# Performance work log

Hardware: AMD Instinct MI355X
Metric: run time of the kernel (lower is better)

## Reference

```python
import jax, jax.numpy as jnp
import numpy as np

B, S, E, H = 8, 1024, 768, 12
D = E // H  # 64


def setup_inputs() -> dict:
    key = jax.random.key(0)
    ks = jax.random.split(key, 9)
    s = 0.02
    hidden_state = jax.random.normal(ks[0], (B, S, E), dtype=jnp.float32)
    # per-head projections stacked: [H, E, D]
    Wq = jax.random.normal(ks[1], (H, E, D), dtype=jnp.float32) * s
    Wk = jax.random.normal(ks[2], (H, E, D), dtype=jnp.float32) * s
    Wv = jax.random.normal(ks[3], (H, E, D), dtype=jnp.float32) * s
    bq = jax.random.normal(ks[4], (H, D), dtype=jnp.float32) * s
    bk = jax.random.normal(ks[5], (H, D), dtype=jnp.float32) * s
    bv = jax.random.normal(ks[6], (H, D), dtype=jnp.float32) * s
    Wo = jax.random.normal(ks[7], (E, E), dtype=jnp.float32) * s
    bo = jax.random.normal(ks[8], (E,), dtype=jnp.float32) * s
    return dict(hidden_state=hidden_state, Wq=Wq, Wk=Wk, Wv=Wv,
                bq=bq, bk=bk, bv=bv, Wo=Wo, bo=bo)


def reference(hidden_state, Wq, Wk, Wv, bq, bk, bv, Wo, bo):
    # project: [B,S,E] x [H,E,D] -> [B,H,S,D]
    q = jnp.einsum('bse,hed->bhsd', hidden_state, Wq) + bq[None, :, None, :]
    k = jnp.einsum('bse,hed->bhsd', hidden_state, Wk) + bk[None, :, None, :]
    v = jnp.einsum('bse,hed->bhsd', hidden_state, Wv) + bv[None, :, None, :]
    scale = 1.0 / jnp.sqrt(jnp.float32(D))
    scores = jnp.einsum('bhsd,bhtd->bhst', q, k) * scale  # [B,H,S,S]
    weights = jax.nn.softmax(scores, axis=-1)
    attn = jnp.einsum('bhst,bhtd->bhsd', weights, v)  # [B,H,S,D]
    # concat heads -> [B,S,E]
    x = attn.transpose(0, 2, 1, 3).reshape(B, S, E)
    return x @ Wo + bo
```

## Files before the change

kernel.cpp:

```cpp
#include <hip/hip_runtime.h>
#include <math.h>

#define BB 8
#define SS 1024
#define EE 768
#define HH 12
#define DD 64

typedef short bf16x8 __attribute__((ext_vector_type(8)));
typedef float f32x4  __attribute__((ext_vector_type(4)));
typedef unsigned short u16x4 __attribute__((ext_vector_type(4)));
typedef unsigned short u16x8 __attribute__((ext_vector_type(8)));

__device__ __forceinline__ unsigned short f2bf(float f) {
    union { float f; unsigned u; } v; v.f = f;
    unsigned r = v.u + 0x7fffu + ((v.u >> 16) & 1u);
    return (unsigned short)(r >> 16);
}

#define SWZ(row, byte) ((byte) ^ (((row) & 7) << 4))

__global__ __launch_bounds__(256) void conv_hs_kernel(
    const float* __restrict__ in, unsigned short* __restrict__ out)
{
    size_t i = ((size_t)blockIdx.x * 256 + threadIdx.x) * 8;
    float4 a = *reinterpret_cast<const float4*>(&in[i]);
    float4 b = *reinterpret_cast<const float4*>(&in[i + 4]);
    u16x8 o;
    o[0] = f2bf(a.x); o[1] = f2bf(a.y); o[2] = f2bf(a.z); o[3] = f2bf(a.w);
    o[4] = f2bf(b.x); o[5] = f2bf(b.y); o[6] = f2bf(b.z); o[7] = f2bf(b.w);
    *reinterpret_cast<u16x8*>(&out[i]) = o;
}

__global__ __launch_bounds__(256) void conv_wqkv_kernel(
    const float* __restrict__ Wq, const float* __restrict__ Wk,
    const float* __restrict__ Wv, unsigned short* __restrict__ WT)
{
    const int z = blockIdx.z;
    const int which = z / HH, h = z - which * HH;
    const float* in = ((which == 0) ? Wq : (which == 1) ? Wk : Wv) + (size_t)h * EE * DD;
    unsigned short* out = WT + (size_t)z * DD * EE;
    const float sc = (which == 0) ? 0.125f : 1.0f;

    __shared__ float t[64][65];
    const int tid = threadIdx.x;
    const int rt0 = blockIdx.x * 64;

    #pragma unroll
    for (int i = 0; i < 16; ++i) {
        int lin = tid + i * 256;
        int r = lin >> 6, c = lin & 63;
        t[r][c] = in[(size_t)(rt0 + r) * DD + c];
    }
    __syncthreads();
    #pragma unroll
    for (int i = 0; i < 16; ++i) {
        int lin = tid + i * 256;
        int c = lin >> 6, r = lin & 63;
        out[(size_t)c * EE + rt0 + r] = f2bf(t[r][c] * sc);
    }
}

__global__ __launch_bounds__(256) void conv_wo_kernel(
    const float* __restrict__ Wo, unsigned short* __restrict__ WoT)
{
    __shared__ float t[64][65];
    const int tid = threadIdx.x;
    const int rt0 = blockIdx.x * 64;
    const int ct0 = blockIdx.y * 64;

    #pragma unroll
    for (int i = 0; i < 16; ++i) {
        int lin = tid + i * 256;
        int r = lin >> 6, c = lin & 63;
        t[r][c] = Wo[(size_t)(rt0 + r) * EE + ct0 + c];
    }
    __syncthreads();
    #pragma unroll
    for (int i = 0; i < 16; ++i) {
        int lin = tid + i * 256;
        int c = lin >> 6, r = lin & 63;
        WoT[(size_t)(ct0 + c) * EE + rt0 + r] = f2bf(t[r][c]);
    }
}

__global__ __launch_bounds__(256) void qkv_mfma_kernel(
    const unsigned short* __restrict__ hsb, const unsigned short* __restrict__ WT,
    const float* __restrict__ bq, const float* __restrict__ bk, const float* __restrict__ bv,
    unsigned short* __restrict__ qo, unsigned short* __restrict__ ko,
    unsigned short* __restrict__ vto)
{
    __shared__ alignas(16) char As[128 * 128];
    __shared__ alignas(16) char Bs[64 * 128];

    const int tid = threadIdx.x;
    const int wv  = tid >> 6;
    const int ln  = tid & 63;
    const int g   = ln >> 4;
    const int lr  = ln & 15;
    const int r0    = blockIdx.x * 128;
    const int h     = blockIdx.y;
    const int which = blockIdx.z;

    const unsigned short* Wt = WT + (size_t)(which * HH + h) * DD * EE;
    const float* bias = (which == 0) ? bq : (which == 1) ? bk : bv;
    const float bsc   = (which == 0) ? 0.125f : 1.0f;

    f32x4 acc[2][4] = {};

    for (int k0 = 0; k0 < EE; k0 += 64) {
        __syncthreads();
        #pragma unroll
        for (int i = 0; i < 4; ++i) {
            int seg = tid + i * 256;
            int row = seg >> 3;
            int sb  = (seg & 7) * 16;
            *reinterpret_cast<bf16x8*>(As + SWZ(row, row * 128 + sb)) =
                *reinterpret_cast<const bf16x8*>(&hsb[(size_t)(r0 + row) * EE + k0 + (seg & 7) * 8]);
        }
        #pragma unroll
        for (int i = 0; i < 2; ++i) {
            int seg = tid + i * 256;
            int row = seg >> 3;
            int sb  = (seg & 7) * 16;
            *reinterpret_cast<bf16x8*>(Bs + SWZ(row, row * 128 + sb)) =
                *reinterpret_cast<const bf16x8*>(&Wt[(size_t)row * EE + k0 + (seg & 7) * 8]);
        }
        __syncthreads();

        #pragma unroll
        for (int c = 0; c < 2; ++c) {
            bf16x8 af[2];
            #pragma unroll
            for (int wr = 0; wr < 2; ++wr) {
                const int arow = wv * 32 + wr * 16 + lr;
                af[wr] = *reinterpret_cast<const bf16x8*>(
                    As + SWZ(arow, arow * 128 + c * 64 + g * 16));
            }
            #pragma unroll
            for (int nf = 0; nf < 4; ++nf) {
                const int bcol = nf * 16 + lr;
                bf16x8 bf = *reinterpret_cast<const bf16x8*>(
                    Bs + SWZ(bcol, bcol * 128 + c * 64 + g * 16));
                #pragma unroll
                for (int wr = 0; wr < 2; ++wr)
                    acc[wr][nf] = __builtin_amdgcn_mfma_f32_16x16x32_bf16(af[wr], bf, acc[wr][nf], 0, 0, 0);
            }
        }
    }

    if (which < 2) {
        unsigned short* C = (which == 0) ? qo : ko;
        #pragma unroll
        for (int nf = 0; nf < 4; ++nf) {
            const int d = nf * 16 + lr;
            const float bia = bias[h * DD + d] * bsc;
            #pragma unroll
            for (int wr = 0; wr < 2; ++wr)
                #pragma unroll
                for (int rr = 0; rr < 4; ++rr) {
                    int row = r0 + wv * 32 + wr * 16 + g * 4 + rr;
                    int b_ = row >> 10, s_ = row & 1023;
                    C[((size_t)(b_ * HH + h) * SS + s_) * DD + d] = f2bf(acc[wr][nf][rr] + bia);
                }
        }
    } else {
        #pragma unroll
        for (int nf = 0; nf < 4; ++nf) {
            const int d = nf * 16 + lr;
            const float bia = bias[h * DD + d];
            #pragma unroll
            for (int wr = 0; wr < 2; ++wr)
                #pragma unroll
                for (int rr = 0; rr < 4; ++rr) {
                    int row = r0 + wv * 32 + wr * 16 + g * 4 + rr;
                    int b_ = row >> 10, s_ = row & 1023;
                    vto[((size_t)(b_ * HH + h) * DD + d) * SS + s_] = f2bf(acc[wr][nf][rr] + bia);
                }
        }
    }
}

__global__ __launch_bounds__(256) void attn_mfma_kernel(
    const unsigned short* __restrict__ qb, const unsigned short* __restrict__ kb,
    const unsigned short* __restrict__ vtb, unsigned short* __restrict__ x)
{
    __shared__ alignas(16) char Ks[64 * 128];
    __shared__ alignas(16) char Vs[64 * 128];
    __shared__ alignas(16) char Pl[4 * 16 * 128];

    const int tid = threadIdx.x;
    const int wv  = tid >> 6;
    const int ln  = tid & 63;
    const int g   = ln >> 4;
    const int lr  = ln & 15;
    const int bh  = blockIdx.y;
    const int qw  = blockIdx.x * 64 + wv * 16;

    const size_t qrow = (size_t)(bh * SS + qw + lr) * DD;
    bf16x8 qf0 = *reinterpret_cast<const bf16x8*>(&qb[qrow + g * 8]);
    bf16x8 qf1 = *reinterpret_cast<const bf16x8*>(&qb[qrow + 32 + g * 8]);

    f32x4 acc_o[4] = {};
    f32x4 lrow = {};

    char* Pw = Pl + wv * 2048;

    for (int t0 = 0; t0 < SS; t0 += 64) {
        __syncthreads();
        #pragma unroll
        for (int i = 0; i < 2; ++i) {
            int c = tid + i * 256;
            int row = c >> 3;
            int seg = c & 7;
            *reinterpret_cast<bf16x8*>(Ks + SWZ(row, row * 128 + seg * 16)) =
                *reinterpret_cast<const bf16x8*>(&kb[(size_t)(bh * SS + t0 + row) * DD + seg * 8]);
            *reinterpret_cast<bf16x8*>(Vs + SWZ(row, row * 128 + seg * 16)) =
                *reinterpret_cast<const bf16x8*>(&vtb[(size_t)(bh * DD + row) * SS + t0 + seg * 8]);
        }
        __syncthreads();

        f32x4 s[4] = {};
        #pragma unroll
        for (int kf = 0; kf < 4; ++kf) {
            int key = kf * 16 + lr;
            bf16x8 k0 = *reinterpret_cast<const bf16x8*>(Ks + SWZ(key, key * 128 + g * 16));
            bf16x8 k1 = *reinterpret_cast<const bf16x8*>(Ks + SWZ(key, key * 128 + 64 + g * 16));
            s[kf] = __builtin_amdgcn_mfma_f32_16x16x32_bf16(qf0, k0, s[kf], 0, 0, 0);
            s[kf] = __builtin_amdgcn_mfma_f32_16x16x32_bf16(qf1, k1, s[kf], 0, 0, 0);
        }

        #pragma unroll
        for (int kf = 0; kf < 4; ++kf)
            #pragma unroll
            for (int r = 0; r < 4; ++r) {
                float p = __expf(s[kf][r]);
                s[kf][r] = p;
                lrow[r] += p;
            }

        #pragma unroll
        for (int kf = 0; kf < 4; ++kf)
            #pragma unroll
            for (int r = 0; r < 4; ++r) {
                int row = g * 4 + r;
                *reinterpret_cast<unsigned short*>(
                    Pw + SWZ(row, row * 128 + (kf * 16 + lr) * 2)) = f2bf(s[kf][r]);
            }

        #pragma unroll
        for (int kk = 0; kk < 2; ++kk) {
            bf16x8 pf8 = *reinterpret_cast<const bf16x8*>(
                Pw + SWZ(lr, lr * 128 + kk * 64 + g * 16));
            #pragma unroll
            for (int nf = 0; nf < 4; ++nf) {
                int d = nf * 16 + lr;
                bf16x8 vf8 = *reinterpret_cast<const bf16x8*>(
                    Vs + SWZ(d, d * 128 + kk * 64 + g * 16));
                acc_o[nf] = __builtin_amdgcn_mfma_f32_16x16x32_bf16(pf8, vf8, acc_o[nf], 0, 0, 0);
            }
        }
    }

    #pragma unroll
    for (int off = 1; off <= 8; off <<= 1)
        #pragma unroll
        for (int r = 0; r < 4; ++r) lrow[r] += __shfl_xor(lrow[r], off, 64);

    const int b_ = bh / HH;
    const int h_ = bh % HH;
    #pragma unroll
    for (int nf = 0; nf < 4; ++nf)
        #pragma unroll
        for (int r = 0; r < 4; ++r) {
            x[(size_t)(b_ * SS + qw + g * 4 + r) * EE + h_ * DD + nf * 16 + lr] =
                f2bf(acc_o[nf][r] / lrow[r]);
        }
}

__global__ __launch_bounds__(256) void out_mfma_kernel(
    const unsigned short* __restrict__ xb, const unsigned short* __restrict__ WoT,
    const float* __restrict__ bo, float* __restrict__ out)
{
    __shared__ alignas(16) char As[64 * 128];
    __shared__ alignas(16) char Bs[64 * 128];

    const int tid = threadIdx.x;
    const int wv  = tid >> 6;
    const int ln  = tid & 63;
    const int g   = ln >> 4;
    const int lr  = ln & 15;
    const int r0  = blockIdx.x * 64;
    const int c0  = blockIdx.y * 64;

    f32x4 acc[4] = {};

    for (int k0 = 0; k0 < EE; k0 += 64) {
        __syncthreads();
        #pragma unroll
        for (int i = 0; i < 2; ++i) {
            int seg = tid + i * 256;
            int row = seg >> 3;
            int sb  = (seg & 7) * 16;
            *reinterpret_cast<bf16x8*>(As + SWZ(row, row * 128 + sb)) =
                *reinterpret_cast<const bf16x8*>(&xb[(size_t)(r0 + row) * EE + k0 + (seg & 7) * 8]);
            *reinterpret_cast<bf16x8*>(Bs + SWZ(row, row * 128 + sb)) =
                *reinterpret_cast<const bf16x8*>(&WoT[(size_t)(c0 + row) * EE + k0 + (seg & 7) * 8]);
        }
        __syncthreads();

        #pragma unroll
        for (int c = 0; c < 2; ++c) {
            const int arow = wv * 16 + lr;
            bf16x8 af = *reinterpret_cast<const bf16x8*>(
                As + SWZ(arow, arow * 128 + c * 64 + g * 16));
            #pragma unroll
            for (int nf = 0; nf < 4; ++nf) {
                const int bcol = nf * 16 + lr;
                bf16x8 bf = *reinterpret_cast<const bf16x8*>(
                    Bs + SWZ(bcol, bcol * 128 + c * 64 + g * 16));
                acc[nf] = __builtin_amdgcn_mfma_f32_16x16x32_bf16(af, bf, acc[nf], 0, 0, 0);
            }
        }
    }

    #pragma unroll
    for (int nf = 0; nf < 4; ++nf) {
        const int d = c0 + nf * 16 + lr;
        const float bia = bo[d];
        #pragma unroll
        for (int rr = 0; rr < 4; ++rr) {
            int row = r0 + wv * 16 + g * 4 + rr;
            out[(size_t)row * EE + d] = acc[nf][rr] + bia;
        }
    }
}

extern "C" void kernel_launch(void* const* d_in, const int* in_sizes, int n_in,
                              void* d_out, int out_size, void* d_ws, size_t ws_size,
                              hipStream_t stream) {
    const float* hs = (const float*)d_in[0];
    const float* Wq = (const float*)d_in[1];
    const float* Wk = (const float*)d_in[2];
    const float* Wv = (const float*)d_in[3];
    const float* bq = (const float*)d_in[4];
    const float* bk = (const float*)d_in[5];
    const float* bv = (const float*)d_in[6];
    const float* Wo = (const float*)d_in[7];
    const float* bo = (const float*)d_in[8];
    float* out = (float*)d_out;

    const size_t per = (size_t)BB * HH * SS * DD;
    unsigned short* qb  = (unsigned short*)d_ws;
    unsigned short* kb  = qb + per;
    unsigned short* vtb = kb + per;
    unsigned short* xb  = vtb + per;
    unsigned short* hsb = xb + per;
    unsigned short* WT  = hsb + per;
    unsigned short* WoT = WT + (size_t)3 * HH * DD * EE;

    conv_hs_kernel<<<dim3(BB * SS * EE / 8 / 256), 256, 0, stream>>>(hs, hsb);
    conv_wqkv_kernel<<<dim3(EE / 64, 1, 3 * HH), 256, 0, stream>>>(Wq, Wk, Wv, WT);
    conv_wo_kernel<<<dim3(EE / 64, EE / 64), 256, 0, stream>>>(Wo, WoT);

    qkv_mfma_kernel<<<dim3(BB * SS / 128, HH, 3), 256, 0, stream>>>(
        hsb, WT, bq, bk, bv, qb, kb, vtb);

    attn_mfma_kernel<<<dim3(SS / 64, BB * HH), 256, 0, stream>>>(qb, kb, vtb, xb);

    out_mfma_kernel<<<dim3(BB * SS / 64, EE / 64), 256, 0, stream>>>(xb, WoT, bo, out);
}
```

Baseline: 237.9 us.

## Enlarge GEMM tiles to 128x128 and process 32 queries per wave in attention

The QKV and output projection kernels switch to 128x128 block tiles with a 2x2 wave grid and 4x4 MFMA accumulators per wave, so each LDS fragment load feeds more MFMAs. The attention kernel gives each wave two 16-row query groups, which halves the K/V tile loads per query and doubles LDS reuse. It also remaps the block index so consecutive blocks group heads per XCD for better L2 locality. In exchange, register and LDS use go up, which may reduce occupancy, and fewer blocks are launched.

```diff
diff --git a/kernel.cpp b/kernel.cpp
--- a/kernel.cpp
+++ b/kernel.cpp
@@ -9,7 +9,6 @@
 
 typedef short bf16x8 __attribute__((ext_vector_type(8)));
 typedef float f32x4  __attribute__((ext_vector_type(4)));
-typedef unsigned short u16x4 __attribute__((ext_vector_type(4)));
 typedef unsigned short u16x8 __attribute__((ext_vector_type(8)));
 
 __device__ __forceinline__ unsigned short f2bf(float f) {
@@ -91,22 +90,19 @@
     unsigned short* __restrict__ vto)
 {
     __shared__ alignas(16) char As[128 * 128];
-    __shared__ alignas(16) char Bs[64 * 128];
+    __shared__ alignas(16) char Bs[128 * 128];
 
     const int tid = threadIdx.x;
     const int wv  = tid >> 6;
     const int ln  = tid & 63;
     const int g   = ln >> 4;
     const int lr  = ln & 15;
-    const int r0    = blockIdx.x * 128;
-    const int h     = blockIdx.y;
-    const int which = blockIdx.z;
-
-    const unsigned short* Wt = WT + (size_t)(which * HH + h) * DD * EE;
-    const float* bias = (which == 0) ? bq : (which == 1) ? bk : bv;
-    const float bsc   = (which == 0) ? 0.125f : 1.0f;
-
-    f32x4 acc[2][4] = {};
+    const int wr  = wv >> 1;
+    const int wc  = wv & 1;
+    const int r0  = blockIdx.x * 128;
+    const int c0  = blockIdx.y * 128;
+
+    f32x4 acc[4][4] = {};
 
     for (int k0 = 0; k0 < EE; k0 += 64) {
         __syncthreads();
@@ -114,40 +110,40 @@
         for (int i = 0; i < 4; ++i) {
             int seg = tid + i * 256;
             int row = seg >> 3;
-            int sb  = (seg & 7) * 16;
-            *reinterpret_cast<bf16x8*>(As + SWZ(row, row * 128 + sb)) =
-                *reinterpret_cast<const bf16x8*>(&hsb[(size_t)(r0 + row) * EE + k0 + (seg & 7) * 8]);
-        }
-        #pragma unroll
-        for (int i = 0; i < 2; ++i) {
-            int seg = tid + i * 256;
-            int row = seg >> 3;
-            int sb  = (seg & 7) * 16;
-            *reinterpret_cast<bf16x8*>(Bs + SWZ(row, row * 128 + sb)) =
-                *reinterpret_cast<const bf16x8*>(&Wt[(size_t)row * EE + k0 + (seg & 7) * 8]);
+            int ch  = seg & 7;
+            *reinterpret_cast<bf16x8*>(As + SWZ(row, row * 128 + ch * 16)) =
+                *reinterpret_cast<const bf16x8*>(&hsb[(size_t)(r0 + row) * EE + k0 + ch * 8]);
+            *reinterpret_cast<bf16x8*>(Bs + SWZ(row, row * 128 + ch * 16)) =
+                *reinterpret_cast<const bf16x8*>(&WT[(size_t)(c0 + row) * EE + k0 + ch * 8]);
         }
         __syncthreads();
 
         #pragma unroll
         for (int c = 0; c < 2; ++c) {
-            bf16x8 af[2];
-            #pragma unroll
-            for (int wr = 0; wr < 2; ++wr) {
-                const int arow = wv * 32 + wr * 16 + lr;
-                af[wr] = *reinterpret_cast<const bf16x8*>(
+            bf16x8 af[4];
+            #pragma unroll
+            for (int m = 0; m < 4; ++m) {
+                const int arow = wr * 64 + m * 16 + lr;
+                af[m] = *reinterpret_cast<const bf16x8*>(
                     As + SWZ(arow, arow * 128 + c * 64 + g * 16));
             }
             #pragma unroll
             for (int nf = 0; nf < 4; ++nf) {
-                const int bcol = nf * 16 + lr;
+                const int bcol = wc * 64 + nf * 16 + lr;
                 bf16x8 bf = *reinterpret_cast<const bf16x8*>(
                     Bs + SWZ(bcol, bcol * 128 + c * 64 + g * 16));
                 #pragma unroll
-                for (int wr = 0; wr < 2; ++wr)
-                    acc[wr][nf] = __builtin_amdgcn_mfma_f32_16x16x32_bf16(af[wr], bf, acc[wr][nf], 0, 0, 0);
-            }
-        }
-    }
+                for (int m = 0; m < 4; ++m)
+                    acc[m][nf] = __builtin_amdgcn_mfma_f32_16x16x32_bf16(af[m], bf, acc[m][nf], 0, 0, 0);
+            }
+        }
+    }
+
+    const int zz    = (c0 + wc * 64) >> 6;
+    const int which = zz / HH;
+    const int h     = zz - which * HH;
+    const float* bias = (which == 0) ? bq : (which == 1) ? bk : bv;
+    const float bsc   = (which == 0) ? 0.125f : 1.0f;
 
     if (which < 2) {
         unsigned short* C = (which == 0) ? qo : ko;
@@ -156,12 +152,12 @@
             const int d = nf * 16 + lr;
             const float bia = bias[h * DD + d] * bsc;
             #pragma unroll
-            for (int wr = 0; wr < 2; ++wr)
+            for (int m = 0; m < 4; ++m)
                 #pragma unroll
                 for (int rr = 0; rr < 4; ++rr) {
-                    int row = r0 + wv * 32 + wr * 16 + g * 4 + rr;
+                    int row = r0 + wr * 64 + m * 16 + g * 4 + rr;
                     int b_ = row >> 10, s_ = row & 1023;
-                    C[((size_t)(b_ * HH + h) * SS + s_) * DD + d] = f2bf(acc[wr][nf][rr] + bia);
+                    C[((size_t)(b_ * HH + h) * SS + s_) * DD + d] = f2bf(acc[m][nf][rr] + bia);
                 }
         }
     } else {
@@ -170,12 +166,12 @@
             const int d = nf * 16 + lr;
             const float bia = bias[h * DD + d];
             #pragma unroll
-            for (int wr = 0; wr < 2; ++wr)
+            for (int m = 0; m < 4; ++m)
                 #pragma unroll
                 for (int rr = 0; rr < 4; ++rr) {
-                    int row = r0 + wv * 32 + wr * 16 + g * 4 + rr;
+                    int row = r0 + wr * 64 + m * 16 + g * 4 + rr;
                     int b_ = row >> 10, s_ = row & 1023;
-                    vto[((size_t)(b_ * HH + h) * DD + d) * SS + s_] = f2bf(acc[wr][nf][rr] + bia);
+                    vto[((size_t)(b_ * HH + h) * DD + d) * SS + s_] = f2bf(acc[m][nf][rr] + bia);
                 }
         }
     }
@@ -187,24 +183,33 @@
 {
     __shared__ alignas(16) char Ks[64 * 128];
     __shared__ alignas(16) char Vs[64 * 128];
-    __shared__ alignas(16) char Pl[4 * 16 * 128];
+    __shared__ alignas(16) char Pl[4 * 32 * 128];
 
     const int tid = threadIdx.x;
     const int wv  = tid >> 6;
     const int ln  = tid & 63;
     const int g   = ln >> 4;
     const int lr  = ln & 15;
-    const int bh  = blockIdx.y;
-    const int qw  = blockIdx.x * 64 + wv * 16;
-
-    const size_t qrow = (size_t)(bh * SS + qw + lr) * DD;
-    bf16x8 qf0 = *reinterpret_cast<const bf16x8*>(&qb[qrow + g * 8]);
-    bf16x8 qf1 = *reinterpret_cast<const bf16x8*>(&qb[qrow + 32 + g * 8]);
-
-    f32x4 acc_o[4] = {};
-    f32x4 lrow = {};
-
-    char* Pw = Pl + wv * 2048;
+
+    const int id = blockIdx.x;
+    const int xc = id & 7;
+    const int j  = id >> 3;
+    const int bh = xc * 12 + (j >> 3);
+    const int qx = j & 7;
+    const int qw = qx * 128 + wv * 32;
+
+    bf16x8 qf[2][2];
+    #pragma unroll
+    for (int w = 0; w < 2; ++w) {
+        const size_t qr = (size_t)(bh * SS + qw + w * 16 + lr) * DD;
+        qf[w][0] = *reinterpret_cast<const bf16x8*>(&qb[qr + g * 8]);
+        qf[w][1] = *reinterpret_cast<const bf16x8*>(&qb[qr + 32 + g * 8]);
+    }
+
+    f32x4 acc_o[2][4] = {};
+    f32x4 lrow[2] = {};
+
+    char* Pw = Pl + wv * 4096;
 
     for (int t0 = 0; t0 < SS; t0 += 64) {
         __syncthreads();
@@ -220,44 +225,49 @@
         }
         __syncthreads();
 
-        f32x4 s[4] = {};
+        f32x4 s[2][4] = {};
         #pragma unroll
         for (int kf = 0; kf < 4; ++kf) {
-            int key = kf * 16 + lr;
+            const int key = kf * 16 + lr;
             bf16x8 k0 = *reinterpret_cast<const bf16x8*>(Ks + SWZ(key, key * 128 + g * 16));
             bf16x8 k1 = *reinterpret_cast<const bf16x8*>(Ks + SWZ(key, key * 128 + 64 + g * 16));
-            s[kf] = __builtin_amdgcn_mfma_f32_16x16x32_bf16(qf0, k0, s[kf], 0, 0, 0);
-            s[kf] = __builtin_amdgcn_mfma_f32_16x16x32_bf16(qf1, k1, s[kf], 0, 0, 0);
-        }
-
-        #pragma unroll
-        for (int kf = 0; kf < 4; ++kf)
-            #pragma unroll
-            for (int r = 0; r < 4; ++r) {
-                float p = __expf(s[kf][r]);
-                s[kf][r] = p;
-                lrow[r] += p;
-            }
-
-        #pragma unroll
-        for (int kf = 0; kf < 4; ++kf)
-            #pragma unroll
-            for (int r = 0; r < 4; ++r) {
-                int row = g * 4 + r;
-                *reinterpret_cast<unsigned short*>(
-                    Pw + SWZ(row, row * 128 + (kf * 16 + lr) * 2)) = f2bf(s[kf][r]);
-            }
+            #pragma unroll
+            for (int w = 0; w < 2; ++w) {
+                s[w][kf] = __builtin_amdgcn_mfma_f32_16x16x32_bf16(qf[w][0], k0, s[w][kf], 0, 0, 0);
+                s[w][kf] = __builtin_amdgcn_mfma_f32_16x16x32_bf16(qf[w][1], k1, s[w][kf], 0, 0, 0);
+            }
+        }
+
+        #pragma unroll
+        for (int w = 0; w < 2; ++w)
+            #pragma unroll
+            for (int kf = 0; kf < 4; ++kf)
+                #pragma unroll
+                for (int r = 0; r < 4; ++r) {
+                    float p = __expf(s[w][kf][r]);
+                    lrow[w][r] += p;
+                    int row = w * 16 + g * 4 + r;
+                    *reinterpret_cast<unsigned short*>(
+                        Pw + SWZ(row, row * 128 + (kf * 16 + lr) * 2)) = f2bf(p);
+                }
 
         #pragma unroll
         for (int kk = 0; kk < 2; ++kk) {
-            bf16x8 pf8 = *reinterpret_cast<const bf16x8*>(
-                Pw + SWZ(lr, lr * 128 + kk * 64 + g * 16));
+            bf16x8 pf[2];
+            #pragma unroll
+            for (int w = 0; w < 2; ++w) {
+                const int prow = w * 16 + lr;
+                pf[w] = *reinterpret_cast<const bf16x8*>(
+                    Pw + SWZ(prow, prow * 128 + kk * 64 + g * 16));
+            }
             #pragma unroll
             for (int nf = 0; nf < 4; ++nf) {
-                int d = nf * 16 + lr;
-                bf16x8 vf8 = *reinterpret_cast<const bf16x8*>(
+                const int d = nf * 16 + lr;
+                bf16x8 vf = *reinterpret_cast<const bf16x8*>(
                     Vs + SWZ(d, d * 128 + kk * 64 + g * 16));
-                acc_o[nf] = __builtin_amdgcn_mfma_f32_16x16x32_bf16(pf8, vf8, acc_o[nf], 0, 0, 0);
+                #pragma unroll
+                for (int w = 0; w < 2; ++w)
+                    acc_o[w][nf] = __builtin_amdgcn_mfma_f32_16x16x32_bf16(pf[w], vf, acc_o[w][nf], 0, 0, 0);
             }
         }
     }
@@ -265,74 +275,88 @@
     #pragma unroll
     for (int off = 1; off <= 8; off <<= 1)
         #pragma unroll
-        for (int r = 0; r < 4; ++r) lrow[r] += __shfl_xor(lrow[r], off, 64);
+        for (int w = 0; w < 2; ++w)
+            #pragma unroll
+            for (int r = 0; r < 4; ++r) lrow[w][r] += __shfl_xor(lrow[w][r], off, 64);
 
     const int b_ = bh / HH;
     const int h_ = bh % HH;
     #pragma unroll
-    for (int nf = 0; nf < 4; ++nf)
-        #pragma unroll
-        for (int r = 0; r < 4; ++r) {
-            x[(size_t)(b_ * SS + qw + g * 4 + r) * EE + h_ * DD + nf * 16 + lr] =
-                f2bf(acc_o[nf][r] / lrow[r]);
-        }
+    for (int w = 0; w < 2; ++w)
+        #pragma unroll
+        for (int nf = 0; nf < 4; ++nf)
+            #pragma unroll
+            for (int r = 0; r < 4; ++r) {
+                x[(size_t)(b_ * SS + qw + w * 16 + g * 4 + r) * EE + h_ * DD + nf * 16 + lr] =
+                    f2bf(acc_o[w][nf][r] / lrow[w][r]);
+            }
 }
 
 __global__ __launch_bounds__(256) void out_mfma_kernel(
     const unsigned short* __restrict__ xb, const unsigned short* __restrict__ WoT,
     const float* __restrict__ bo, float* __restrict__ out)
 {
-    __shared__ alignas(16) char As[64 * 128];
-    __shared__ alignas(16) char Bs[64 * 128];
+    __shared__ alignas(16) char As[128 * 128];
+    __shared__ alignas(16) char Bs[128 * 128];
 
     const int tid = threadIdx.x;
     const int wv  = tid >> 6;
     const int ln  = tid & 63;
     const int g   = ln >> 4;
     const int lr  = ln & 15;
-    const int r0  = blockIdx.x * 64;
-    const int c0  = blockIdx.y * 64;
-
-    f32x4 acc[4] = {};
+    const int wr  = wv >> 1;
+    const int wc  = wv & 1;
+    const int r0  = blockIdx.x * 128;
+    const int c0  = blockIdx.y * 128;
+
+    f32x4 acc[4][4] = {};
 
     for (int k0 = 0; k0 < EE; k0 += 64) {
         __syncthreads();
         #pragma unroll
-        for (int i = 0; i < 2; ++i) {
+        for (int i = 0; i < 4; ++i) {
             int seg = tid + i * 256;
             int row = seg >> 3;
-            int sb  = (seg & 7) * 16;
-            *reinterpret_cast<bf16x8*>(As + SWZ(row, row * 128 + sb)) =
-                *reinterpret_cast<const bf16x8*>(&xb[(size_t)(r0 + row) * EE + k0 + (seg & 7) * 8]);
-            *reinterpret_cast<bf16x8*>(Bs + SWZ(row, row * 128 + sb)) =
-                *reinterpret_cast<const bf16x8*>(&WoT[(size_t)(c0 + row) * EE + k0 + (seg & 7) * 8]);
+            int ch  = seg & 7;
+            *reinterpret_cast<bf16x8*>(As + SWZ(row, row * 128 + ch * 16)) =
+                *reinterpret_cast<const bf16x8*>(&xb[(size_t)(r0 + row) * EE + k0 + ch * 8]);
+            *reinterpret_cast<bf16x8*>(Bs + SWZ(row, row * 128 + ch * 16)) =
+                *reinterpret_cast<const bf16x8*>(&WoT[(size_t)(c0 + row) * EE + k0 + ch * 8]);
         }
         __syncthreads();
 
         #pragma unroll
         for (int c = 0; c < 2; ++c) {
-            const int arow = wv * 16 + lr;
-            bf16x8 af = *reinterpret_cast<const bf16x8*>(
-                As + SWZ(arow, arow * 128 + c * 64 + g * 16));
+            bf16x8 af[4];
+            #pragma unroll
+            for (int m = 0; m < 4; ++m) {
+                const int arow = wr * 64 + m * 16 + lr;
+                af[m] = *reinterpret_cast<const bf16x8*>(
+                    As + SWZ(arow, arow * 128 + c * 64 + g * 16));
+            }
             #pragma unroll
             for (int nf = 0; nf < 4; ++nf) {
-                const int bcol = nf * 16 + lr;
+                const int bcol = wc * 64 + nf * 16 + lr;
                 bf16x8 bf = *reinterpret_cast<const bf16x8*>(
                     Bs + SWZ(bcol, bcol * 128 + c * 64 + g * 16));
-                acc[nf] = __builtin_amdgcn_mfma_f32_16x16x32_bf16(af, bf, acc[nf], 0, 0, 0);
+                #pragma unroll
+                for (int m = 0; m < 4; ++m)
+                    acc[m][nf] = __builtin_amdgcn_mfma_f32_16x16x32_bf16(af[m], bf, acc[m][nf], 0, 0, 0);
             }
         }
     }
 
     #pragma unroll
     for (int nf = 0; nf < 4; ++nf) {
-        const int d = c0 + nf * 16 + lr;
-        const float bia = bo[d];
-        #pragma unroll
-        for (int rr = 0; rr < 4; ++rr) {
-            int row = r0 + wv * 16 + g * 4 + rr;
-            out[(size_t)row * EE + d] = acc[nf][rr] + bia;
-        }
+        const int col = c0 + wc * 64 + nf * 16 + lr;
+        const float bia = bo[col];
+        #pragma unroll
+        for (int m = 0; m < 4; ++m)
+            #pragma unroll
+            for (int rr = 0; rr < 4; ++rr) {
+                int row = r0 + wr * 64 + m * 16 + g * 4 + rr;
+                out[(size_t)row * EE + col] = acc[m][nf][rr] + bia;
+            }
     }
 }
 
@@ -363,10 +387,10 @@
     conv_wqkv_kernel<<<dim3(EE / 64, 1, 3 * HH), 256, 0, stream>>>(Wq, Wk, Wv, WT);
     conv_wo_kernel<<<dim3(EE / 64, EE / 64), 256, 0, stream>>>(Wo, WoT);
 
-    qkv_mfma_kernel<<<dim3(BB * SS / 128, HH, 3), 256, 0, stream>>>(
+    qkv_mfma_kernel<<<dim3(BB * SS / 128, 3 * HH * DD / 128), 256, 0, stream>>>(
         hsb, WT, bq, bk, bv, qb, kb, vtb);
 
-    attn_mfma_kernel<<<dim3(SS / 64, BB * HH), 256, 0, stream>>>(qb, kb, vtb, xb);
-
-    out_mfma_kernel<<<dim3(BB * SS / 64, EE / 64), 256, 0, stream>>>(xb, WoT, bo, out);
-}
+    attn_mfma_kernel<<<dim3((SS / 128) * BB * HH), 256, 0, stream>>>(qb, kb, vtb, xb);
+
+    out_mfma_kernel<<<dim3(BB * SS / 128, EE / 128), 256, 0, stream>>>(xb, WoT, bo, out);
+}
```

After: 229.1 us. 3.7% less time.
